# Performance work log

Hardware: AMD Instinct MI355X
Metric: run time of the kernel (lower is better)

The kernel has to match this reference:

```python
import jax, jax.numpy as jnp
import numpy as np

H = 1024      # hidden_size
NH = 16       # num_heads
HD = H // NH  # head_dim


def setup_inputs() -> dict:
    key = jax.random.key(0)
    ks = jax.random.split(key, 5)
    x = jax.random.normal(ks[0], (2, 2048, H), dtype=jnp.float32)
    # nn.Linear weights are [out, in]; keep that convention
    w_qkv = jax.random.normal(ks[1], (3 * H, H), dtype=jnp.float32) * (1.0 / np.sqrt(H))
    b_qkv = jax.random.normal(ks[2], (3 * H,), dtype=jnp.float32) * 0.01
    w_out = jax.random.normal(ks[3], (H, H), dtype=jnp.float32) * (1.0 / np.sqrt(H))
    b_out = jax.random.normal(ks[4], (H,), dtype=jnp.float32) * 0.01
    return {"x": x, "w_qkv": w_qkv, "b_qkv": b_qkv, "w_out": w_out, "b_out": b_out}


def reference(x, w_qkv, b_qkv, w_out, b_out):
    B, L, _ = x.shape
    scale = HD ** -0.5
    qkv = x @ w_qkv.T + b_qkv                       # [B,L,3H]
    qkv = qkv.reshape(B, L, 3, NH, HD).transpose(2, 0, 3, 1, 4)  # [3,B,NH,L,HD]
    q, k, v = qkv[0], qkv[1], qkv[2]
    attn = jnp.einsum('bhqd,bhkd->bhqk', q, k) * scale
    attn = jax.nn.softmax(attn, axis=-1)            # dropout is identity in eval
    out = jnp.einsum('bhqk,bhkd->bhqd', attn, v)    # [B,NH,L,HD]
    out = out.transpose(0, 2, 1, 3).reshape(B, L, H)
    return out @ w_out.T + b_out
```

## Files before the change

### kernel.cpp

```cpp
#include <hip/hip_runtime.h>
#include <hip/hip_bf16.h>
#include <stdint.h>

#define H_DIM  1024
#define NHEADS 16
#define HDIM   64
#define BATCH  2
#define SEQ    2048
#define MROWS  (BATCH * SEQ)
#define QKV_N  (3 * H_DIM)
#define QK_LD  (2 * H_DIM)
#define NT     (SEQ / 64)

typedef __attribute__((ext_vector_type(8))) __bf16 bf16x8;
typedef __attribute__((ext_vector_type(4))) float  floatx4;

__device__ __forceinline__ unsigned short f2bf(float f) {
    uint32_t u = __float_as_uint(f);
    u += 0x7fffu + ((u >> 16) & 1u);
    return (unsigned short)(u >> 16);
}
__device__ __forceinline__ float bf2f(unsigned short u) {
    return __uint_as_float(((uint32_t)u) << 16);
}
__device__ __forceinline__ uint32_t cvtpk_bf16(float lo, float hi) {
    uint32_t r;
    asm("v_cvt_pk_bf16_f32 %0, %1, %2" : "=v"(r) : "v"(lo), "v"(hi));
    return r;
}

#if __has_builtin(__builtin_amdgcn_exp2f)
#define fexp2 __builtin_amdgcn_exp2f
#else
#define fexp2 exp2f
#endif

__device__ __forceinline__ void async_ld16(const void* g, void* l) {
    __builtin_amdgcn_global_load_lds(
        (const __attribute__((address_space(1))) void*)g,
        (__attribute__((address_space(3))) void*)l, 16, 0, 0);
}

#define N4_X   (MROWS * H_DIM / 4)
#define N4_WQ  (QKV_N * H_DIM / 4)
#define N4_WO  (H_DIM * H_DIM / 4)
__global__ __launch_bounds__(256) void cvt_all(const float4* __restrict__ x,
                                               const float4* __restrict__ wq,
                                               const float4* __restrict__ wo,
                                               ushort4* __restrict__ xb,
                                               ushort4* __restrict__ wqb,
                                               ushort4* __restrict__ wob) {
    int i = blockIdx.x * 256 + threadIdx.x;
    const float4* in;
    ushort4* out;
    int j;
    if (i < N4_X)                { in = x;  out = xb;  j = i; }
    else if (i < N4_X + N4_WQ)   { in = wq; out = wqb; j = i - N4_X; }
    else                         { in = wo; out = wob; j = i - N4_X - N4_WQ; }
    float4 v = in[j];
    ushort4 o;
    o.x = f2bf(v.x); o.y = f2bf(v.y); o.z = f2bf(v.z); o.w = f2bf(v.w);
    out[j] = o;
}

__global__ __launch_bounds__(256) void transpose_v(const unsigned short* __restrict__ vr,
                                                   unsigned short* __restrict__ vt) {
    __shared__ unsigned short T[64][72];
    const int tid = threadIdx.x;
    const int bh = blockIdx.y;
    const int b = bh >> 4, h = bh & 15;
    const int kv0 = blockIdx.x * 64;
    const int r  = tid >> 2, cs = (tid & 3) * 16;

    const unsigned short* src = &vr[(size_t)(b * SEQ + kv0 + r) * H_DIM + h * HDIM + cs];
    union { uint4 q; unsigned short u[8]; } A0, A1;
    A0.q = *(const uint4*)&src[0];
    A1.q = *(const uint4*)&src[8];
    #pragma unroll
    for (int e = 0; e < 8; ++e) T[cs + e][r]     = A0.u[e];
    #pragma unroll
    for (int e = 0; e < 8; ++e) T[cs + 8 + e][r] = A1.u[e];
    __syncthreads();

    const int dd = tid >> 2, ks = (tid & 3) * 16;
    unsigned short* dst = &vt[((size_t)bh * HDIM + dd) * SEQ + kv0 + ks];
    *(uint4*)&dst[0] = *(const uint4*)&T[dd][ks];
    *(uint4*)&dst[8] = *(const uint4*)&T[dd][ks + 8];
}

__global__ __launch_bounds__(256) void gemm_bt(const unsigned short* __restrict__ A,
                                               const unsigned short* __restrict__ B,
                                               const float* __restrict__ bias,
                                               unsigned short* __restrict__ Cb,
                                               float* __restrict__ Cf,
                                               unsigned short* __restrict__ Vr,
                                               int ldc, int Kdim) {
    __shared__ __align__(16) unsigned short As[128 * 64];
    __shared__ __align__(16) unsigned short Bs[128 * 64];
    const int tid  = threadIdx.x;
    const int lane = tid & 63;
    const int wave = tid >> 6;
    const int waveM = (wave >> 1) * 64;
    const int waveN = (wave & 1) * 64;

    const int nwg = gridDim.x * gridDim.y;
    int wg = blockIdx.y * gridDim.x + blockIdx.x;
    wg = (wg & 7) * (nwg >> 3) + (wg >> 3);
    const int bm = wg / gridDim.x, bn = wg % gridDim.x;

    floatx4 acc[4][4];
    #pragma unroll
    for (int i = 0; i < 4; ++i)
        #pragma unroll
        for (int j = 0; j < 4; ++j) {
            floatx4 z = {0.f, 0.f, 0.f, 0.f};
            acc[i][j] = z;
        }

    const unsigned short* pA[4];
    const unsigned short* pB[4];
    #pragma unroll
    for (int i = 0; i < 4; ++i) {
        int c = i * 256 + tid;
        int row = c >> 3;
        int kc  = ((c & 7) ^ (row & 7)) * 8;
        pA[i] = A + (size_t)(bm * 128 + row) * Kdim + kc;
        pB[i] = B + (size_t)(bn * 128 + row) * Kdim + kc;
    }

    const int lr = lane & 15;
    const int g  = lane >> 4;
    const int sw = lr & 7;

    for (int k0 = 0; k0 < Kdim; k0 += 64) {
        #pragma unroll
        for (int i = 0; i < 4; ++i) {
            async_ld16(pA[i], (char*)As + i * 4096 + wave * 1024);
            async_ld16(pB[i], (char*)Bs + i * 4096 + wave * 1024);
            pA[i] += 64; pB[i] += 64;
        }
        __syncthreads();

        #pragma unroll
        for (int kk = 0; kk < 2; ++kk) {
            const int gk = (((kk << 2) + g) ^ sw) * 8;
            bf16x8 af[4], bfr[4];
            #pragma unroll
            for (int i = 0; i < 4; ++i)
                af[i] = *(const bf16x8*)&As[(waveM + i * 16 + lr) * 64 + gk];
            #pragma unroll
            for (int j = 0; j < 4; ++j)
                bfr[j] = *(const bf16x8*)&Bs[(waveN + j * 16 + lr) * 64 + gk];

            #pragma unroll
            for (int i = 0; i < 4; ++i)
                #pragma unroll
                for (int j = 0; j < 4; ++j)
                    acc[i][j] = __builtin_amdgcn_mfma_f32_16x16x32_bf16(af[i], bfr[j], acc[i][j], 0, 0, 0);
        }
        __syncthreads();
    }

    const int crow0 = bm * 128 + waveM + (lane >> 4) * 4;
    const int ccol0 = bn * 128 + waveN + (lane & 15);
    #pragma unroll
    for (int i = 0; i < 4; ++i)
        #pragma unroll
        for (int j = 0; j < 4; ++j) {
            int col = ccol0 + j * 16;
            float bv = bias[col];
            #pragma unroll
            for (int r = 0; r < 4; ++r) {
                int row = crow0 + i * 16 + r;
                float v = acc[i][j][r] + bv;
                if (Vr && col >= 2 * H_DIM) {
                    Vr[(size_t)row * H_DIM + (col - 2 * H_DIM)] = f2bf(v);
                } else if (Cb) {
                    Cb[(size_t)row * ldc + col] = f2bf(v);
                } else {
                    Cf[(size_t)row * ldc + col] = v;
                }
            }
        }
}

__global__ __launch_bounds__(256) void gemm_bt64(const unsigned short* __restrict__ A,
                                                 const unsigned short* __restrict__ B,
                                                 const float* __restrict__ bias,
                                                 float* __restrict__ Cf,
                                                 int ldc, int Kdim) {
    __shared__ __align__(16) unsigned short As[128 * 64];
    __shared__ __align__(16) unsigned short Bs[64 * 64];
    const int tid  = threadIdx.x;
    const int lane = tid & 63;
    const int wave = tid >> 6;
    const int waveM = wave * 32;

    const int nwg = gridDim.x * gridDim.y;
    int wg = blockIdx.y * gridDim.x + blockIdx.x;
    wg = (wg & 7) * (nwg >> 3) + (wg >> 3);
    const int bm = wg / gridDim.x, bn = wg % gridDim.x;

    floatx4 acc[2][4];
    #pragma unroll
    for (int i = 0; i < 2; ++i)
        #pragma unroll
        for (int j = 0; j < 4; ++j) {
            floatx4 z = {0.f, 0.f, 0.f, 0.f};
            acc[i][j] = z;
        }

    const unsigned short* pA[4];
    const unsigned short* pB[2];
    #pragma unroll
    for (int i = 0; i < 4; ++i) {
        int c = i * 256 + tid;
        int row = c >> 3;
        int kc  = ((c & 7) ^ (row & 7)) * 8;
        pA[i] = A + (size_t)(bm * 128 + row) * Kdim + kc;
        if (i < 2) pB[i] = B + (size_t)(bn * 64 + row) * Kdim + kc;
    }

    const int lr = lane & 15;
    const int g  = lane >> 4;
    const int sw = lr & 7;

    for (int k0 = 0; k0 < Kdim; k0 += 64) {
        #pragma unroll
        for (int i = 0; i < 4; ++i) {
            async_ld16(pA[i], (char*)As + i * 4096 + wave * 1024);
            pA[i] += 64;
        }
        #pragma unroll
        for (int i = 0; i < 2; ++i) {
            async_ld16(pB[i], (char*)Bs + i * 4096 + wave * 1024);
            pB[i] += 64;
        }
        __syncthreads();

        #pragma unroll
        for (int kk = 0; kk < 2; ++kk) {
            const int gk = (((kk << 2) + g) ^ sw) * 8;
            bf16x8 af[2], bfr[4];
            #pragma unroll
            for (int i = 0; i < 2; ++i)
                af[i] = *(const bf16x8*)&As[(waveM + i * 16 + lr) * 64 + gk];
            #pragma unroll
            for (int j = 0; j < 4; ++j)
                bfr[j] = *(const bf16x8*)&Bs[(j * 16 + lr) * 64 + gk];

            #pragma unroll
            for (int i = 0; i < 2; ++i)
                #pragma unroll
                for (int j = 0; j < 4; ++j)
                    acc[i][j] = __builtin_amdgcn_mfma_f32_16x16x32_bf16(af[i], bfr[j], acc[i][j], 0, 0, 0);
        }
        __syncthreads();
    }

    const int crow0 = bm * 128 + waveM + (lane >> 4) * 4;
    const int ccol0 = bn * 64 + (lane & 15);
    #pragma unroll
    for (int i = 0; i < 2; ++i)
        #pragma unroll
        for (int j = 0; j < 4; ++j) {
            int col = ccol0 + j * 16;
            float bv = bias[col];
            #pragma unroll
            for (int r = 0; r < 4; ++r) {
                int row = crow0 + i * 16 + r;
                Cf[(size_t)row * ldc + col] = acc[i][j][r] + bv;
            }
        }
}

__global__ __launch_bounds__(256, 2) void attn_mfma(const unsigned short* __restrict__ qkv2,
                                                    const unsigned short* __restrict__ vt,
                                                    unsigned short* __restrict__ ctx) {
    __shared__ __align__(16) unsigned short Ks2[2][64 * 64];
    __shared__ __align__(16) unsigned short Vt2[2][64 * 64];

    const int tid  = threadIdx.x;
    const int lane = tid & 63;
    const int wave = tid >> 6;

    const int f  = blockIdx.y * gridDim.x + blockIdx.x;
    const int bh = ((f >> 7) << 3) + (f & 7);
    const int qt = (f >> 3) & 15;
    const int b  = bh >> 4, h = bh & 15;
    const int q0 = qt * 128 + wave * 32;
    const int lq = lane & 15;
    const int g  = lane >> 4;
    const int swz = lq & 7;

    const float QS = 0.125f * 1.44269504f;
    bf16x8 qf[2][2];
    #pragma unroll
    for (int s = 0; s < 2; ++s)
        #pragma unroll
        for (int kk = 0; kk < 2; ++kk) {
            union { bf16x8 v; unsigned short u[8]; } tq;
            tq.v = *(const bf16x8*)&qkv2[(size_t)(b * SEQ + q0 + s * 16 + lq) * QK_LD
                                         + h * HDIM + kk * 32 + g * 8];
            #pragma unroll
            for (int e = 0; e < 8; ++e) tq.u[e] = f2bf(bf2f(tq.u[e]) * QS);
            qf[s][kk] = tq.v;
        }

    floatx4 acc_o[2][4];
    #pragma unroll
    for (int s = 0; s < 2; ++s)
        #pragma unroll
        for (int j = 0; j < 4; ++j) {
            floatx4 z = {0.f, 0.f, 0.f, 0.f};
            acc_o[s][j] = z;
        }
    float l_run[2] = {0.f, 0.f};

    const unsigned short* gK = qkv2 + (size_t)b * SEQ * QK_LD + H_DIM + (size_t)h * HDIM;
    const unsigned short* gV = vt + (size_t)bh * HDIM * SEQ;

    const int r0  = tid >> 3;
    const int pr0 = (r0 & 32) | ((r0 & 12) << 1) | ((r0 & 16) >> 2) | (r0 & 3);
    const int gs0 = (tid & 7) ^ (r0 & 7);
    const unsigned short* pK0 = gK + (size_t)pr0 * QK_LD + gs0 * 8;
    const unsigned short* pK1 = gK + (size_t)(pr0 + 32) * QK_LD + gs0 * 8;
    const unsigned short* pV0 = gV + (size_t)r0 * SEQ + gs0 * 8;
    const unsigned short* pV1 = gV + (size_t)(r0 + 32) * SEQ + gs0 * 8;

    #define STAGE_KV(bi)                                                        \
        {                                                                       \
            async_ld16(pK0, (char*)&Ks2[bi][0] + (wave * 64) * 16);             \
            async_ld16(pK1, (char*)&Ks2[bi][0] + (256 + wave * 64) * 16);       \
            async_ld16(pV0, (char*)&Vt2[bi][0] + (wave * 64) * 16);             \
            async_ld16(pV1, (char*)&Vt2[bi][0] + (256 + wave * 64) * 16);       \
            pK0 += 64 * QK_LD; pK1 += 64 * QK_LD; pV0 += 64; pV1 += 64;         \
        }

    STAGE_KV(0)
    __syncthreads();

    int buf = 0;
    for (int t = 0; t < NT; ++t) {
        if (t + 1 < NT) STAGE_KV(buf ^ 1)

        const unsigned short* Ksb = &Ks2[buf][0];
        const unsigned short* Vsb = &Vt2[buf][0];

        bf16x8 kf[4][2];
        #pragma unroll
        for (int jb = 0; jb < 4; ++jb)
            #pragma unroll
            for (int kk = 0; kk < 2; ++kk)
                kf[jb][kk] = *(const bf16x8*)&Ksb[(jb * 16 + lq) * 64 + (((kk << 2) + g) ^ swz) * 8];

        bf16x8 vf[4][2];
        #pragma unroll
        for (int dt = 0; dt < 4; ++dt)
            #pragma unroll
            for (int kk = 0; kk < 2; ++kk)
                vf[dt][kk] = *(const bf16x8*)&Vsb[(dt * 16 + lq) * 64 + (((kk << 2) + g) ^ swz) * 8];

        __builtin_amdgcn_sched_barrier(0);

        floatx4 sa[2][4];
        #pragma unroll
        for (int s = 0; s < 2; ++s)
            #pragma unroll
            for (int jb = 0; jb < 4; ++jb) {
                floatx4 z = {0.f, 0.f, 0.f, 0.f};
                sa[s][jb] = z;
            }
        __builtin_amdgcn_s_setprio(1);
        #pragma unroll
        for (int s = 0; s < 2; ++s)
            #pragma unroll
            for (int jb = 0; jb < 4; ++jb)
                #pragma unroll
                for (int kk = 0; kk < 2; ++kk)
                    sa[s][jb] = __builtin_amdgcn_mfma_f32_16x16x32_bf16(kf[jb][kk], qf[s][kk], sa[s][jb], 0, 0, 0);
        __builtin_amdgcn_s_setprio(0);

        #pragma unroll
        for (int s = 0; s < 2; ++s) {
            float ps = 0.f;
            {
                float e00 = fexp2(sa[s][0][0]), e01 = fexp2(sa[s][0][1]), e02 = fexp2(sa[s][0][2]), e03 = fexp2(sa[s][0][3]);
                float e10 = fexp2(sa[s][1][0]), e11 = fexp2(sa[s][1][1]), e12 = fexp2(sa[s][1][2]), e13 = fexp2(sa[s][1][3]);
                ps += ((e00 + e01) + (e02 + e03)) + ((e10 + e11) + (e12 + e13));
                union { bf16x8 v; uint32_t u[4]; } pf;
                pf.u[0] = cvtpk_bf16(e00, e01); pf.u[1] = cvtpk_bf16(e02, e03);
                pf.u[2] = cvtpk_bf16(e10, e11); pf.u[3] = cvtpk_bf16(e12, e13);
                __builtin_amdgcn_s_setprio(1);
                #pragma unroll
                for (int dt = 0; dt < 4; ++dt)
                    acc_o[s][dt] = __builtin_amdgcn_mfma_f32_16x16x32_bf16(pf.v, vf[dt][0], acc_o[s][dt], 0, 0, 0);
                __builtin_amdgcn_s_setprio(0);
            }
            {
                float e00 = fexp2(sa[s][2][0]), e01 = fexp2(sa[s][2][1]), e02 = fexp2(sa[s][2][2]), e03 = fexp2(sa[s][2][3]);
                float e10 = fexp2(sa[s][3][0]), e11 = fexp2(sa[s][3][1]), e12 = fexp2(sa[s][3][2]), e13 = fexp2(sa[s][3][3]);
                ps += ((e00 + e01) + (e02 + e03)) + ((e10 + e11) + (e12 + e13));
                union { bf16x8 v; uint32_t u[4]; } pf;
                pf.u[0] = cvtpk_bf16(e00, e01); pf.u[1] = cvtpk_bf16(e02, e03);
                pf.u[2] = cvtpk_bf16(e10, e11); pf.u[3] = cvtpk_bf16(e12, e13);
                __builtin_amdgcn_s_setprio(1);
                #pragma unroll
                for (int dt = 0; dt < 4; ++dt)
                    acc_o[s][dt] = __builtin_amdgcn_mfma_f32_16x16x32_bf16(pf.v, vf[dt][1], acc_o[s][dt], 0, 0, 0);
                __builtin_amdgcn_s_setprio(0);
            }
            ps += __shfl_xor(ps, 16);
            ps += __shfl_xor(ps, 32);
            l_run[s] += ps;
        }

        __syncthreads();
        buf ^= 1;
    }
    #undef STAGE_KV

    #pragma unroll
    for (int s = 0; s < 2; ++s) {
        float linv[4];
        #pragma unroll
        for (int r = 0; r < 4; ++r)
            linv[r] = 1.f / __shfl(l_run[s], g * 4 + r);
        #pragma unroll
        for (int dt = 0; dt < 4; ++dt)
            #pragma unroll
            for (int r = 0; r < 4; ++r)
                ctx[(size_t)(b * SEQ + q0 + s * 16 + g * 4 + r) * H_DIM + h * HDIM + dt * 16 + lq]
                    = f2bf(acc_o[s][dt][r] * linv[r]);
    }
}

extern "C" void kernel_launch(void* const* d_in, const int* in_sizes, int n_in,
                              void* d_out, int out_size, void* d_ws, size_t ws_size,
                              hipStream_t stream) {
    const float* x     = (const float*)d_in[0];
    const float* w_qkv = (const float*)d_in[1];
    const float* b_qkv = (const float*)d_in[2];
    const float* w_out = (const float*)d_in[3];
    const float* b_out = (const float*)d_in[4];
    float* out = (float*)d_out;

    unsigned short* xb    = (unsigned short*)d_ws;
    unsigned short* wqkvb = xb    + (size_t)MROWS * H_DIM;
    unsigned short* woutb = wqkvb + (size_t)QKV_N * H_DIM;
    unsigned short* qkv2  = woutb + (size_t)H_DIM * H_DIM;
    unsigned short* ctxb  = qkv2  + (size_t)MROWS * QK_LD;
    unsigned short* vtb   = ctxb  + (size_t)MROWS * H_DIM;
    unsigned short* vrows = ctxb;

    cvt_all<<<(N4_X + N4_WQ + N4_WO) / 256, 256, 0, stream>>>(
        (const float4*)x, (const float4*)w_qkv, (const float4*)w_out,
        (ushort4*)xb, (ushort4*)wqkvb, (ushort4*)woutb);

    gemm_bt<<<dim3(QKV_N / 128, MROWS / 128), 256, 0, stream>>>(
        xb, wqkvb, b_qkv, qkv2, nullptr, vrows, QK_LD, H_DIM);

    transpose_v<<<dim3(SEQ / 64, BATCH * NHEADS), 256, 0, stream>>>(vrows, vtb);

    attn_mfma<<<dim3(SEQ / 128, BATCH * NHEADS), 256, 0, stream>>>(qkv2, vtb, ctxb);

    gemm_bt64<<<dim3(H_DIM / 64, MROWS / 128), 256, 0, stream>>>(
        ctxb, woutb, b_out, out, H_DIM, H_DIM);
}
```

Measured before the change: 186.6 us.

## Double-buffer QKV GEMM K-loop with async LDS prefetch; grid-stride conversion kernel

The QKV projection GEMM now splits K into 32-wide stages held in two LDS buffers. The next stage's global-to-LDS async loads are issued before computing on the current one, and partial vmcnt waits plus raw barriers replace the old load-then-sync loop. The LDS swizzle is reworked for the 32-wide rows. Separately, the fp32-to-bf16 conversion kernel switches to a fixed 2048-block grid-stride loop. The aim is to hide global load latency behind the MFMAs, at the cost of twice as many barriers per K step and half the MFMA work per stage.

```diff
diff --git a/kernel.cpp b/kernel.cpp
--- a/kernel.cpp
+++ b/kernel.cpp
@@ -44,23 +44,25 @@
 #define N4_X   (MROWS * H_DIM / 4)
 #define N4_WQ  (QKV_N * H_DIM / 4)
 #define N4_WO  (H_DIM * H_DIM / 4)
+#define N4_TOT (N4_X + N4_WQ + N4_WO)
 __global__ __launch_bounds__(256) void cvt_all(const float4* __restrict__ x,
                                                const float4* __restrict__ wq,
                                                const float4* __restrict__ wo,
                                                ushort4* __restrict__ xb,
                                                ushort4* __restrict__ wqb,
                                                ushort4* __restrict__ wob) {
-    int i = blockIdx.x * 256 + threadIdx.x;
-    const float4* in;
-    ushort4* out;
-    int j;
-    if (i < N4_X)                { in = x;  out = xb;  j = i; }
-    else if (i < N4_X + N4_WQ)   { in = wq; out = wqb; j = i - N4_X; }
-    else                         { in = wo; out = wob; j = i - N4_X - N4_WQ; }
-    float4 v = in[j];
-    ushort4 o;
-    o.x = f2bf(v.x); o.y = f2bf(v.y); o.z = f2bf(v.z); o.w = f2bf(v.w);
-    out[j] = o;
+    for (int i = blockIdx.x * 256 + threadIdx.x; i < N4_TOT; i += gridDim.x * 256) {
+        const float4* in;
+        ushort4* out;
+        int j;
+        if (i < N4_X)                { in = x;  out = xb;  j = i; }
+        else if (i < N4_X + N4_WQ)   { in = wq; out = wqb; j = i - N4_X; }
+        else                         { in = wo; out = wob; j = i - N4_X - N4_WQ; }
+        float4 v = in[j];
+        ushort4 o;
+        o.x = f2bf(v.x); o.y = f2bf(v.y); o.z = f2bf(v.z); o.w = f2bf(v.w);
+        out[j] = o;
+    }
 }
 
 __global__ __launch_bounds__(256) void transpose_v(const unsigned short* __restrict__ vr,
@@ -95,8 +97,8 @@
                                                float* __restrict__ Cf,
                                                unsigned short* __restrict__ Vr,
                                                int ldc, int Kdim) {
-    __shared__ __align__(16) unsigned short As[128 * 64];
-    __shared__ __align__(16) unsigned short Bs[128 * 64];
+    __shared__ __align__(16) unsigned short As2[2][128 * 32];
+    __shared__ __align__(16) unsigned short Bs2[2][128 * 32];
     const int tid  = threadIdx.x;
     const int lane = tid & 63;
     const int wave = tid >> 6;
@@ -117,49 +119,63 @@
             acc[i][j] = z;
         }
 
-    const unsigned short* pA[4];
-    const unsigned short* pB[4];
-    #pragma unroll
-    for (int i = 0; i < 4; ++i) {
+    const unsigned short* pA[2];
+    const unsigned short* pB[2];
+    #pragma unroll
+    for (int i = 0; i < 2; ++i) {
         int c = i * 256 + tid;
-        int row = c >> 3;
-        int kc  = ((c & 7) ^ (row & 7)) * 8;
+        int row = c >> 2;
+        int kc  = (((c & 3) ^ (row & 3) ^ ((row >> 2) & 3))) * 8;
         pA[i] = A + (size_t)(bm * 128 + row) * Kdim + kc;
         pB[i] = B + (size_t)(bn * 128 + row) * Kdim + kc;
     }
 
     const int lr = lane & 15;
     const int g  = lane >> 4;
-    const int sw = lr & 7;
-
-    for (int k0 = 0; k0 < Kdim; k0 += 64) {
-        #pragma unroll
-        for (int i = 0; i < 4; ++i) {
-            async_ld16(pA[i], (char*)As + i * 4096 + wave * 1024);
-            async_ld16(pB[i], (char*)Bs + i * 4096 + wave * 1024);
-            pA[i] += 64; pB[i] += 64;
-        }
-        __syncthreads();
-
-        #pragma unroll
-        for (int kk = 0; kk < 2; ++kk) {
-            const int gk = (((kk << 2) + g) ^ sw) * 8;
-            bf16x8 af[4], bfr[4];
-            #pragma unroll
-            for (int i = 0; i < 4; ++i)
-                af[i] = *(const bf16x8*)&As[(waveM + i * 16 + lr) * 64 + gk];
+    const int pgx = (lr & 3) ^ ((lr >> 2) & 3);
+
+    #define STAGEG(bi)                                                  \
+        {                                                               \
+            _Pragma("unroll")                                           \
+            for (int i = 0; i < 2; ++i) {                               \
+                async_ld16(pA[i], (char*)As2[bi] + i * 4096 + wave * 1024); \
+                async_ld16(pB[i], (char*)Bs2[bi] + i * 4096 + wave * 1024); \
+                pA[i] += 32; pB[i] += 32;                               \
+            }                                                           \
+        }
+
+    STAGEG(0)
+
+    int buf = 0;
+    const int nst = Kdim / 32;
+    for (int st = 0; st < nst; ++st) {
+        if (st + 1 < nst) {
+            STAGEG(buf ^ 1)
+            asm volatile("s_waitcnt vmcnt(4)" ::: "memory");
+        } else {
+            asm volatile("s_waitcnt vmcnt(0)" ::: "memory");
+        }
+        __builtin_amdgcn_s_barrier();
+
+        const int gk = (g ^ pgx) * 8;
+        bf16x8 af[4], bfr[4];
+        #pragma unroll
+        for (int i = 0; i < 4; ++i)
+            af[i] = *(const bf16x8*)&As2[buf][(waveM + i * 16 + lr) * 32 + gk];
+        #pragma unroll
+        for (int j = 0; j < 4; ++j)
+            bfr[j] = *(const bf16x8*)&Bs2[buf][(waveN + j * 16 + lr) * 32 + gk];
+
+        #pragma unroll
+        for (int i = 0; i < 4; ++i)
             #pragma unroll
             for (int j = 0; j < 4; ++j)
-                bfr[j] = *(const bf16x8*)&Bs[(waveN + j * 16 + lr) * 64 + gk];
-
-            #pragma unroll
-            for (int i = 0; i < 4; ++i)
-                #pragma unroll
-                for (int j = 0; j < 4; ++j)
-                    acc[i][j] = __builtin_amdgcn_mfma_f32_16x16x32_bf16(af[i], bfr[j], acc[i][j], 0, 0, 0);
-        }
-        __syncthreads();
-    }
+                acc[i][j] = __builtin_amdgcn_mfma_f32_16x16x32_bf16(af[i], bfr[j], acc[i][j], 0, 0, 0);
+
+        __builtin_amdgcn_s_barrier();
+        buf ^= 1;
+    }
+    #undef STAGEG
 
     const int crow0 = bm * 128 + waveM + (lane >> 4) * 4;
     const int ccol0 = bn * 128 + waveN + (lane & 15);
@@ -453,7 +469,7 @@
     unsigned short* vtb   = ctxb  + (size_t)MROWS * H_DIM;
     unsigned short* vrows = ctxb;
 
-    cvt_all<<<(N4_X + N4_WQ + N4_WO) / 256, 256, 0, stream>>>(
+    cvt_all<<<2048, 256, 0, stream>>>(
         (const float4*)x, (const float4*)w_qkv, (const float4*)w_out,
         (ushort4*)xb, (ushort4*)wqkvb, (ushort4*)woutb);
 
```

Result: no change. 185.7 us (-0.5%).
